# Kernel tuning notes

Measured on AMD Instinct MI355X. Metric: run time of the kernel, lower is better.

Reference implementation:

```python
import jax, jax.numpy as jnp
import numpy as np

CLAMP = 60.0
EPS = 1e-4

def _make_weights(N, alpha_logits, delta_logits, beta_logits):
    alpha = jax.nn.sigmoid(alpha_logits)   # [C,H]
    delta = jax.nn.sigmoid(delta_logits)
    beta = jax.nn.sigmoid(beta_logits)
    A = alpha * beta                        # [C,H]
    r = jnp.clip(1.0 - alpha * delta, EPS, 1.0 - EPS)
    t = jnp.arange(N, dtype=jnp.float32)[:, None, None]   # [N,1,1]
    logr = jnp.clip(jnp.log(r) * t, -CLAMP, CLAMP)        # [N,C,H]
    return A, jnp.exp(logr), jnp.exp(-logr)

def _ema_fwd(x, A, eta, r_pos, r_neg):
    # x: [B,N,C] -> y: [B,N,C]
    z = A * x[..., None] * r_neg            # [B,N,C,H]
    h = jnp.cumsum(z, axis=1) * r_pos       # [B,N,C,H]
    return jnp.sum(eta * h, axis=-1)        # [B,N,C]

def reference(x, alpha_logits, delta_logits, beta_logits, eta, proj_w, proj_b):
    B, N, C = x.shape
    A, r_pos, r_neg = _make_weights(N, alpha_logits, delta_logits, beta_logits)
    xf = x.astype(jnp.float32)
    y_fwd = _ema_fwd(xf, A, eta, r_pos, r_neg)
    y_bwd = _ema_fwd(xf[:, ::-1], A, eta, r_pos, r_neg)[:, ::-1]
    z = jnp.concatenate([y_fwd, y_bwd], axis=-1).astype(x.dtype)  # [B,N,2C]
    return z @ proj_w.T + proj_b            # [B,N,C]

def setup_inputs():
    key = jax.random.key(0)
    ks = jax.random.split(key, 7)
    B, N, C, H = 8, 4096, 512, 4
    return {
        "x": jax.random.normal(ks[0], (B, N, C), dtype=jnp.float32),
        "alpha_logits": jax.random.normal(ks[1], (C, H), dtype=jnp.float32),
        "delta_logits": jax.random.normal(ks[2], (C, H), dtype=jnp.float32),
        "beta_logits": jax.random.normal(ks[3], (C, H), dtype=jnp.float32),
        "eta": jax.random.normal(ks[4], (C, H), dtype=jnp.float32) * 0.02,
        "proj_w": jax.random.normal(ks[5], (C, 2 * C), dtype=jnp.float32) / np.sqrt(2.0 * C),
        "proj_b": jax.random.normal(ks[6], (C,), dtype=jnp.float32) * 0.01,
    }
```

## Files before the change

kernel.cpp:

```cpp
#include <hip/hip_runtime.h>
#include <hip/hip_bf16.h>

#define B_ 8
#define N_ 4096
#define C_ 512
#define H_ 4
#define EPS_ 1e-4f
#define E60P 1.14200739e26f
#define E60M 8.7565108e-27f

typedef __attribute__((ext_vector_type(8))) short short8;
typedef __attribute__((ext_vector_type(4))) float floatx4;
typedef __attribute__((ext_vector_type(2))) float floatx2;
typedef unsigned short ushort_t;

__device__ __forceinline__ float sigmoidf_(float v) {
    return 1.0f / (1.0f + expf(-v));
}

__device__ __forceinline__ int pk_off(int t, int w, int k0, int ks, int f,
                                      int lane8, int kb) {
    return ((((t * 2 + w) * 16 + k0) * 2 + ks) * 4 + f) * 512 + lane8 * 8 + kb;
}

__global__ __launch_bounds__(256) void k_partials3(
    const float* __restrict__ x, const float* __restrict__ al,
    const float* __restrict__ dl, const float* __restrict__ bl,
    float* __restrict__ P)
{
    int bid   = blockIdx.x;
    int chunk = bid & 15;
    int ct    = (bid >> 4) & 7;
    int b     = bid >> 7;
    int lane  = threadIdx.x & 63;
    int wave  = threadIdx.x >> 6;
    int c     = ct * 64 + lane;
    int sub   = chunk * 4 + wave;
    int t0f   = sub * 64;
    int t0b   = (63 - sub) * 64;

    float aa[4], dd[4], bb[4];
    { float4 v = ((const float4*)al)[c]; aa[0]=v.x; aa[1]=v.y; aa[2]=v.z; aa[3]=v.w; }
    { float4 v = ((const float4*)dl)[c]; dd[0]=v.x; dd[1]=v.y; dd[2]=v.z; dd[3]=v.w; }
    { float4 v = ((const float4*)bl)[c]; bb[0]=v.x; bb[1]=v.y; bb[2]=v.z; bb[3]=v.w; }

    float A[H_], ri[H_], Lh[H_];
    #pragma unroll
    for (int h = 0; h < H_; ++h) {
        float alpha = sigmoidf_(aa[h]);
        float delta = sigmoidf_(dd[h]);
        float beta  = sigmoidf_(bb[h]);
        A[h] = alpha * beta;
        float r = fminf(fmaxf(1.0f - alpha * delta, EPS_), 1.0f - EPS_);
        Lh[h] = logf(r);
        ri[h] = 1.0f / r;
    }
    const floatx2 E2P = {E60P, E60P};
    floatx2 A2[2]  = {{A[0],  A[1]},  {A[2],  A[3]}};
    floatx2 ri2[2] = {{ri[0], ri[1]}, {ri[2], ri[3]}};

    const float* xp = x + ((size_t)b * N_ + t0f) * C_ + c;

    floatx2 ep2[2], T2[2];
    #pragma unroll
    for (int p = 0; p < 2; ++p) {
        ep2[p] = (floatx2){expf(fminf(-Lh[2*p]   * (float)t0f, 60.0f)),
                           expf(fminf(-Lh[2*p+1] * (float)t0f, 60.0f))};
        T2[p]  = (floatx2){0.f, 0.f};
    }
    {
        float cur[8];
        #pragma unroll
        for (int j = 0; j < 8; ++j) cur[j] = xp[(size_t)j * C_];
        #pragma unroll 1
        for (int g = 0; g < 8; ++g) {
            float nxt[8];
            if (g < 7) {
                #pragma unroll
                for (int j = 0; j < 8; ++j)
                    nxt[j] = xp[(size_t)(g * 8 + 8 + j) * C_];
            }
            #pragma unroll
            for (int j = 0; j < 8; ++j) {
                floatx2 xv2 = {cur[j], cur[j]};
                #pragma unroll
                for (int p = 0; p < 2; ++p) {
                    T2[p] += (A2[p] * xv2) * ep2[p];
                    ep2[p] = __builtin_elementwise_min(ep2[p] * ri2[p], E2P);
                }
            }
            if (g < 7) {
                #pragma unroll
                for (int j = 0; j < 8; ++j) cur[j] = nxt[j];
            }
        }
        float* pp = P + ((size_t)b * 64 + sub) * (H_ * C_) + c;
        pp[0]      = T2[0].x;  pp[C_]     = T2[0].y;
        pp[2 * C_] = T2[1].x;  pp[3 * C_] = T2[1].y;
    }

    #pragma unroll
    for (int p = 0; p < 2; ++p) {
        ep2[p] = (floatx2){expf(fminf(-Lh[2*p]   * (float)t0b, 60.0f)),
                           expf(fminf(-Lh[2*p+1] * (float)t0b, 60.0f))};
        T2[p]  = (floatx2){0.f, 0.f};
    }
    {
        float cur[8];
        #pragma unroll
        for (int j = 0; j < 8; ++j) cur[j] = xp[(size_t)(63 - j) * C_];
        #pragma unroll 1
        for (int g = 0; g < 8; ++g) {
            float nxt[8];
            if (g < 7) {
                #pragma unroll
                for (int j = 0; j < 8; ++j)
                    nxt[j] = xp[(size_t)(63 - (g * 8 + 8 + j)) * C_];
            }
            #pragma unroll
            for (int j = 0; j < 8; ++j) {
                floatx2 xv2 = {cur[j], cur[j]};
                #pragma unroll
                for (int p = 0; p < 2; ++p) {
                    T2[p] += (A2[p] * xv2) * ep2[p];
                    ep2[p] = __builtin_elementwise_min(ep2[p] * ri2[p], E2P);
                }
            }
            if (g < 7) {
                #pragma unroll
                for (int j = 0; j < 8; ++j) cur[j] = nxt[j];
            }
        }
        float* pp = P + ((size_t)(8 + b) * 64 + (63 - sub)) * (H_ * C_) + c;
        pp[0]      = T2[0].x;  pp[C_]     = T2[0].y;
        pp[2 * C_] = T2[1].x;  pp[3 * C_] = T2[1].y;
    }
}

__global__ __launch_bounds__(256) void k_scan(float* __restrict__ P)
{
    int bid = blockIdx.x;
    int ct  = bid & 7;
    int b   = (bid >> 3) & 7;
    int dir = bid >> 6;
    int cl  = threadIdx.x & 63;
    int h   = threadIdx.x >> 6;
    int c   = ct * 64 + cl;

    float run = 0.0f;
    float* base = P + ((size_t)(dir * 8 + b) * 64) * (H_ * C_) + h * C_ + c;
    for (int s = 0; s < 64; ++s) {
        float v = base[s * (H_ * C_)];
        base[s * (H_ * C_)] = run;
        run += v;
    }
}

__global__ __launch_bounds__(256) void k_apply3(
    const float* __restrict__ x, const float* __restrict__ al,
    const float* __restrict__ dl, const float* __restrict__ bl,
    const float* __restrict__ eta, const float* __restrict__ P,
    ushort_t* __restrict__ Zp)
{
    int bid   = blockIdx.x;
    int chunk = bid & 15;
    int ct    = (bid >> 4) & 7;
    int b     = bid >> 7;
    int lane  = threadIdx.x & 63;
    int wave  = threadIdx.x >> 6;
    int c     = ct * 64 + lane;
    int sub   = chunk * 4 + wave;
    int t0f   = sub * 64;
    int t0b   = (63 - sub) * 64;

    int ksv = lane >> 5, qv = (lane >> 3) & 3, kbv = lane & 7;
    int mt  = b * 32 + (t0f >> 7);
    int wq  = (t0f >> 6) & 1;
    int offcF = pk_off(mt, wq, ct,     ksv, 0, qv * 16, kbv);
    int offcB = pk_off(mt, wq, 8 + ct, ksv, 0, qv * 16, kbv);

    float aa[4], dd[4], bb[4], ee[4];
    { float4 v = ((const float4*)al )[c]; aa[0]=v.x; aa[1]=v.y; aa[2]=v.z; aa[3]=v.w; }
    { float4 v = ((const float4*)dl )[c]; dd[0]=v.x; dd[1]=v.y; dd[2]=v.z; dd[3]=v.w; }
    { float4 v = ((const float4*)bl )[c]; bb[0]=v.x; bb[1]=v.y; bb[2]=v.z; bb[3]=v.w; }
    { float4 v = ((const float4*)eta)[c]; ee[0]=v.x; ee[1]=v.y; ee[2]=v.z; ee[3]=v.w; }

    float A[H_], rr[H_], ri[H_], Lh[H_];
    #pragma unroll
    for (int h = 0; h < H_; ++h) {
        float alpha = sigmoidf_(aa[h]);
        float delta = sigmoidf_(dd[h]);
        float beta  = sigmoidf_(bb[h]);
        A[h] = alpha * beta;
        float r = fminf(fmaxf(1.0f - alpha * delta, EPS_), 1.0f - EPS_);
        Lh[h] = logf(r);
        rr[h] = r;
        ri[h] = 1.0f / r;
    }
    const floatx2 E2P = {E60P, E60P};
    const floatx2 E2M = {E60M, E60M};
    floatx2 A2[2]  = {{A[0],  A[1]},  {A[2],  A[3]}};
    floatx2 ri2[2] = {{ri[0], ri[1]}, {ri[2], ri[3]}};
    floatx2 rr2[2] = {{rr[0], rr[1]}, {rr[2], rr[3]}};
    floatx2 ee2[2] = {{ee[0], ee[1]}, {ee[2], ee[3]}};

    const float* xp = x + ((size_t)b * N_ + t0f) * C_ + c;

    {
        const float* cp = P + ((size_t)b * 64 + sub) * (H_ * C_) + c;
        floatx2 ep2[2], em2[2], S2[2];
        #pragma unroll
        for (int p = 0; p < 2; ++p) {
            ep2[p] = (floatx2){expf(fminf(-Lh[2*p]   * (float)t0f, 60.0f)),
                               expf(fminf(-Lh[2*p+1] * (float)t0f, 60.0f))};
            em2[p] = (floatx2){expf(fmaxf( Lh[2*p]   * (float)t0f, -60.0f)),
                               expf(fmaxf( Lh[2*p+1] * (float)t0f, -60.0f))};
            S2[p]  = (floatx2){cp[(2*p) * C_], cp[(2*p+1) * C_]};
        }
        float cur[8];
        #pragma unroll
        for (int j = 0; j < 8; ++j) cur[j] = xp[(size_t)j * C_];
        #pragma unroll 1
        for (int g = 0; g < 8; ++g) {
            float nxt[8];
            if (g < 7) {
                #pragma unroll
                for (int j = 0; j < 8; ++j)
                    nxt[j] = xp[(size_t)(g * 8 + 8 + j) * C_];
            }
            #pragma unroll
            for (int j = 0; j < 8; ++j) {
                int i = g * 8 + j;
                floatx2 xv2 = {cur[j], cur[j]};
                floatx2 acc = {0.f, 0.f};
                #pragma unroll
                for (int p = 0; p < 2; ++p) {
                    S2[p] += (A2[p] * xv2) * ep2[p];
                    ep2[p] = __builtin_elementwise_min(ep2[p] * ri2[p], E2P);
                    acc   += ee2[p] * (em2[p] * S2[p]);
                    em2[p] = __builtin_elementwise_max(em2[p] * rr2[p], E2M);
                }
                float y = acc.x + acc.y;
                __hip_bfloat16 yb = __float2bfloat16(y);
                Zp[offcF + (i >> 4) * 512 + (i & 15) * 8] = *(ushort_t*)&yb;
            }
            if (g < 7) {
                #pragma unroll
                for (int j = 0; j < 8; ++j) cur[j] = nxt[j];
            }
        }
    }

    {
        const float* cp = P + ((size_t)(8 + b) * 64 + (63 - sub)) * (H_ * C_) + c;
        floatx2 ep2[2], em2[2], S2[2];
        #pragma unroll
        for (int p = 0; p < 2; ++p) {
            ep2[p] = (floatx2){expf(fminf(-Lh[2*p]   * (float)t0b, 60.0f)),
                               expf(fminf(-Lh[2*p+1] * (float)t0b, 60.0f))};
            em2[p] = (floatx2){expf(fmaxf( Lh[2*p]   * (float)t0b, -60.0f)),
                               expf(fmaxf( Lh[2*p+1] * (float)t0b, -60.0f))};
            S2[p]  = (floatx2){cp[(2*p) * C_], cp[(2*p+1) * C_]};
        }
        float cur[8];
        #pragma unroll
        for (int j = 0; j < 8; ++j) cur[j] = xp[(size_t)(63 - j) * C_];
        #pragma unroll 1
        for (int g = 0; g < 8; ++g) {
            float nxt[8];
            if (g < 7) {
                #pragma unroll
                for (int j = 0; j < 8; ++j)
                    nxt[j] = xp[(size_t)(63 - (g * 8 + 8 + j)) * C_];
            }
            #pragma unroll
            for (int j = 0; j < 8; ++j) {
                int i = 63 - (g * 8 + j);
                floatx2 xv2 = {cur[j], cur[j]};
                floatx2 acc = {0.f, 0.f};
                #pragma unroll
                for (int p = 0; p < 2; ++p) {
                    S2[p] += (A2[p] * xv2) * ep2[p];
                    ep2[p] = __builtin_elementwise_min(ep2[p] * ri2[p], E2P);
                    acc   += ee2[p] * (em2[p] * S2[p]);
                    em2[p] = __builtin_elementwise_max(em2[p] * rr2[p], E2M);
                }
                float y = acc.x + acc.y;
                __hip_bfloat16 yb = __float2bfloat16(y);
                Zp[offcB + (i >> 4) * 512 + (i & 15) * 8] = *(ushort_t*)&yb;
            }
            if (g < 7) {
                #pragma unroll
                for (int j = 0; j < 8; ++j) cur[j] = nxt[j];
            }
        }
    }
}

__global__ __launch_bounds__(256) void k_cvtw2(const float* __restrict__ w,
                                               ushort_t* __restrict__ Wp)
{
    int i = blockIdx.x * 256 + threadIdx.x;
    int n = i >> 10, k = i & 1023;
    int nt = n >> 7, rn = n & 127;
    int k0 = k >> 6, kk = k & 63;
    int off = pk_off(nt, rn >> 6, k0, kk >> 5, (rn >> 4) & 3,
                     ((kk >> 3) & 3) * 16 + (rn & 15), kk & 7);
    __hip_bfloat16 vb = __float2bfloat16(w[i]);
    Wp[off] = *(ushort_t*)&vb;
}

__global__ __launch_bounds__(256, 2) void k_gemm2(
    const ushort_t* __restrict__ Zp, const ushort_t* __restrict__ Wp,
    const float* __restrict__ bias, float* __restrict__ out)
{
    __shared__ __align__(16) float stg[32 * 132];

    int tid  = threadIdx.x;
    int lane = tid & 63, wave = tid >> 6;
    int wm   = wave & 1, wn = wave >> 1;
    int fr   = lane & 15, quad = lane >> 4;

    int bid = blockIdx.x;
    int mt  = ((bid >> 5) << 3) | (bid & 7);
    int nt  = (bid >> 3) & 3;
    int m0  = mt * 128, n0 = nt * 128;

    const ushort_t* Ab = Zp + ((size_t)(mt * 2 + wm) * 16) * 4096 + lane * 8;
    const ushort_t* Bb = Wp + ((size_t)(nt * 2 + wn) * 16) * 4096 + lane * 8;

    floatx4 acc[4][4];
    #pragma unroll
    for (int mf = 0; mf < 4; ++mf)
        #pragma unroll
        for (int nf = 0; nf < 4; ++nf)
            acc[mf][nf] = (floatx4){0.f, 0.f, 0.f, 0.f};

    #pragma unroll
    for (int k0 = 0; k0 < 16; ++k0) {
        short8 af[2][4], bf[2][4];
        #pragma unroll
        for (int ks = 0; ks < 2; ++ks)
            #pragma unroll
            for (int f = 0; f < 4; ++f) {
                af[ks][f] = *(const short8*)(Ab + k0 * 4096 + (ks * 4 + f) * 512);
                bf[ks][f] = *(const short8*)(Bb + k0 * 4096 + (ks * 4 + f) * 512);
            }
        #pragma unroll
        for (int ks = 0; ks < 2; ++ks)
            #pragma unroll
            for (int mf = 0; mf < 4; ++mf)
                #pragma unroll
                for (int nf = 0; nf < 4; ++nf)
                    acc[mf][nf] = __builtin_amdgcn_mfma_f32_16x16x32_bf16(
                        af[ks][mf], bf[ks][nf], acc[mf][nf], 0, 0, 0);
    }

    int rrow = tid >> 3;
    int seg  = tid & 7;
    int gcol = n0 + seg * 16;

    #pragma unroll
    for (int ch = 0; ch < 4; ++ch) {
        if ((wave & 1) == (ch >> 1)) {
            int ml = (ch & 1) * 2;
            #pragma unroll
            for (int mi = 0; mi < 2; ++mi) {
                #pragma unroll
                for (int nf = 0; nf < 4; ++nf) {
                    int col = wn * 64 + nf * 16 + fr;
                    #pragma unroll
                    for (int rg = 0; rg < 4; ++rg) {
                        int row = mi * 16 + quad * 4 + rg;
                        stg[row * 132 + col] = acc[ml + mi][nf][rg];
                    }
                }
            }
        }
        __syncthreads();
        {
            int gm = m0 + ch * 32 + rrow;
            const float* s = &stg[rrow * 132 + seg * 16];
            #pragma unroll
            for (int k = 0; k < 4; ++k) {
                float4 v  = *(const float4*)&s[k * 4];
                float4 bv = *(const float4*)&bias[gcol + k * 4];
                v.x += bv.x; v.y += bv.y; v.z += bv.z; v.w += bv.w;
                *(float4*)&out[(size_t)gm * 512 + gcol + k * 4] = v;
            }
        }
        __syncthreads();
    }
}

extern "C" void kernel_launch(void* const* d_in, const int* in_sizes, int n_in,
                              void* d_out, int out_size, void* d_ws, size_t ws_size,
                              hipStream_t stream)
{
    const float* x  = (const float*)d_in[0];
    const float* al = (const float*)d_in[1];
    const float* dl = (const float*)d_in[2];
    const float* bl = (const float*)d_in[3];
    const float* et = (const float*)d_in[4];
    const float* pw = (const float*)d_in[5];
    const float* pb = (const float*)d_in[6];
    float* out = (float*)d_out;

    ushort_t* Zp = (ushort_t*)d_ws;
    float*    P  = (float*)((char*)d_ws + 67108864);
    ushort_t* Wp = (ushort_t*)((char*)d_ws + 75497472);

    hipLaunchKernelGGL(k_cvtw2,     dim3(2048), dim3(256), 0, stream, pw, Wp);
    hipLaunchKernelGGL(k_partials3, dim3(1024), dim3(256), 0, stream, x, al, dl, bl, P);
    hipLaunchKernelGGL(k_scan,      dim3(128),  dim3(256), 0, stream, P);
    hipLaunchKernelGGL(k_apply3,    dim3(1024), dim3(256), 0, stream, x, al, dl, bl, et, P, Zp);
    hipLaunchKernelGGL(k_gemm2,     dim3(1024), dim3(256), 0, stream, Zp, Wp, pb, out);
}
```

Baseline: 225.1 us.

## Stage GEMM operands via global_load_lds, vectorize weight convert, batch scan loads

The GEMM now copies each K-slab of A and B into shared memory with direct global-to-LDS loads, so each tile is fetched once per block rather than once per wave. It synchronizes twice per K-step and raises the occupancy hint to 4 blocks per CU. The weight conversion kernel now handles four elements per thread with float4 loads and 64-bit stores. The scan kernel loads all 64 partials into registers before running the prefix sum, which removes the serialized load-store dependency. Single-buffered LDS staging with a full vmcnt wait can expose memory latency, since no copy overlaps the MFMA work.

```diff
diff --git a/kernel.cpp b/kernel.cpp
--- a/kernel.cpp
+++ b/kernel.cpp
@@ -12,6 +12,7 @@
 typedef __attribute__((ext_vector_type(8))) short short8;
 typedef __attribute__((ext_vector_type(4))) float floatx4;
 typedef __attribute__((ext_vector_type(2))) float floatx2;
+typedef __attribute__((ext_vector_type(4))) unsigned short ushort4_t;
 typedef unsigned short ushort_t;
 
 __device__ __forceinline__ float sigmoidf_(float v) {
@@ -21,6 +22,12 @@
 __device__ __forceinline__ int pk_off(int t, int w, int k0, int ks, int f,
                                       int lane8, int kb) {
     return ((((t * 2 + w) * 16 + k0) * 2 + ks) * 4 + f) * 512 + lane8 * 8 + kb;
+}
+
+__device__ __forceinline__ void gload16(const void* g, void* l) {
+    __builtin_amdgcn_global_load_lds(
+        (const __attribute__((address_space(1))) void*)g,
+        (__attribute__((address_space(3))) void*)l, 16, 0, 0);
 }
 
 __global__ __launch_bounds__(256) void k_partials3(
@@ -147,13 +154,18 @@
     int h   = threadIdx.x >> 6;
     int c   = ct * 64 + cl;
 
+    float* base = P + ((size_t)(dir * 8 + b) * 64) * (H_ * C_) + h * C_ + c;
+
+    float v[64];
+    #pragma unroll
+    for (int s = 0; s < 64; ++s) v[s] = base[s * (H_ * C_)];
+
     float run = 0.0f;
-    float* base = P + ((size_t)(dir * 8 + b) * 64) * (H_ * C_) + h * C_ + c;
-    for (int s = 0; s < 64; ++s) {
-        float v = base[s * (H_ * C_)];
-        base[s * (H_ * C_)] = run;
-        run += v;
-    }
+    #pragma unroll
+    for (int s = 0; s < 64; ++s) { float t = v[s]; v[s] = run; run += t; }
+
+    #pragma unroll
+    for (int s = 0; s < 64; ++s) base[s * (H_ * C_)] = v[s];
 }
 
 __global__ __launch_bounds__(256) void k_apply3(
@@ -300,21 +312,30 @@
 __global__ __launch_bounds__(256) void k_cvtw2(const float* __restrict__ w,
                                                ushort_t* __restrict__ Wp)
 {
-    int i = blockIdx.x * 256 + threadIdx.x;
+    int i4 = blockIdx.x * 256 + threadIdx.x;
+    int i  = i4 << 2;
     int n = i >> 10, k = i & 1023;
     int nt = n >> 7, rn = n & 127;
     int k0 = k >> 6, kk = k & 63;
     int off = pk_off(nt, rn >> 6, k0, kk >> 5, (rn >> 4) & 3,
                      ((kk >> 3) & 3) * 16 + (rn & 15), kk & 7);
-    __hip_bfloat16 vb = __float2bfloat16(w[i]);
-    Wp[off] = *(ushort_t*)&vb;
-}
-
-__global__ __launch_bounds__(256, 2) void k_gemm2(
+    float4 v = ((const float4*)w)[i4];
+    ushort4_t r;
+    { __hip_bfloat16 t = __float2bfloat16(v.x); r.x = *(ushort_t*)&t; }
+    { __hip_bfloat16 t = __float2bfloat16(v.y); r.y = *(ushort_t*)&t; }
+    { __hip_bfloat16 t = __float2bfloat16(v.z); r.z = *(ushort_t*)&t; }
+    { __hip_bfloat16 t = __float2bfloat16(v.w); r.w = *(ushort_t*)&t; }
+    *(ushort4_t*)&Wp[off] = r;
+}
+
+__global__ __launch_bounds__(256, 4) void k_gemm3(
     const ushort_t* __restrict__ Zp, const ushort_t* __restrict__ Wp,
     const float* __restrict__ bias, float* __restrict__ out)
 {
-    __shared__ __align__(16) float stg[32 * 132];
+    __shared__ __align__(16) char lds[32768];
+    char*  ldsA = lds;
+    char*  ldsB = lds + 16384;
+    float* stg  = (float*)lds;
 
     int tid  = threadIdx.x;
     int lane = tid & 63, wave = tid >> 6;
@@ -326,8 +347,8 @@
     int nt  = (bid >> 3) & 3;
     int m0  = mt * 128, n0 = nt * 128;
 
-    const ushort_t* Ab = Zp + ((size_t)(mt * 2 + wm) * 16) * 4096 + lane * 8;
-    const ushort_t* Bb = Wp + ((size_t)(nt * 2 + wn) * 16) * 4096 + lane * 8;
+    const ushort_t* Az = Zp + ((size_t)(mt * 2) * 16) * 4096;
+    const ushort_t* Bz = Wp + ((size_t)(nt * 2) * 16) * 4096;
 
     floatx4 acc[4][4];
     #pragma unroll
@@ -336,24 +357,37 @@
         for (int nf = 0; nf < 4; ++nf)
             acc[mf][nf] = (floatx4){0.f, 0.f, 0.f, 0.f};
 
-    #pragma unroll
     for (int k0 = 0; k0 < 16; ++k0) {
-        short8 af[2][4], bf[2][4];
-        #pragma unroll
-        for (int ks = 0; ks < 2; ++ks)
+        const ushort_t* As = Az + (size_t)k0 * 4096;
+        const ushort_t* Bs = Bz + (size_t)k0 * 4096;
+        #pragma unroll
+        for (int w = 0; w < 2; ++w)
+            #pragma unroll
+            for (int inst = 0; inst < 2; ++inst) {
+                gload16(As + w * 65536 + inst * 2048 + tid * 8,
+                        ldsA + w * 8192 + inst * 4096 + tid * 16);
+                gload16(Bs + w * 65536 + inst * 2048 + tid * 8,
+                        ldsB + w * 8192 + inst * 4096 + tid * 16);
+            }
+        asm volatile("s_waitcnt vmcnt(0)" ::: "memory");
+        __syncthreads();
+
+        #pragma unroll
+        for (int ks = 0; ks < 2; ++ks) {
+            short8 af[4], bf[4];
             #pragma unroll
             for (int f = 0; f < 4; ++f) {
-                af[ks][f] = *(const short8*)(Ab + k0 * 4096 + (ks * 4 + f) * 512);
-                bf[ks][f] = *(const short8*)(Bb + k0 * 4096 + (ks * 4 + f) * 512);
-            }
-        #pragma unroll
-        for (int ks = 0; ks < 2; ++ks)
+                af[f] = *(const short8*)(ldsA + wm * 8192 + (ks * 4 + f) * 1024 + lane * 16);
+                bf[f] = *(const short8*)(ldsB + wn * 8192 + (ks * 4 + f) * 1024 + lane * 16);
+            }
             #pragma unroll
             for (int mf = 0; mf < 4; ++mf)
                 #pragma unroll
                 for (int nf = 0; nf < 4; ++nf)
                     acc[mf][nf] = __builtin_amdgcn_mfma_f32_16x16x32_bf16(
-                        af[ks][mf], bf[ks][nf], acc[mf][nf], 0, 0, 0);
+                        af[mf], bf[nf], acc[mf][nf], 0, 0, 0);
+        }
+        __syncthreads();
     }
 
     int rrow = tid >> 3;
@@ -410,9 +444,9 @@
     float*    P  = (float*)((char*)d_ws + 67108864);
     ushort_t* Wp = (ushort_t*)((char*)d_ws + 75497472);
 
-    hipLaunchKernelGGL(k_cvtw2,     dim3(2048), dim3(256), 0, stream, pw, Wp);
+    hipLaunchKernelGGL(k_cvtw2,     dim3(512),  dim3(256), 0, stream, pw, Wp);
     hipLaunchKernelGGL(k_partials3, dim3(1024), dim3(256), 0, stream, x, al, dl, bl, P);
     hipLaunchKernelGGL(k_scan,      dim3(128),  dim3(256), 0, stream, P);
     hipLaunchKernelGGL(k_apply3,    dim3(1024), dim3(256), 0, stream, x, al, dl, bl, et, P, Zp);
-    hipLaunchKernelGGL(k_gemm2,     dim3(1024), dim3(256), 0, stream, Zp, Wp, pb, out);
-}
+    hipLaunchKernelGGL(k_gemm3,     dim3(1024), dim3(256), 0, stream, Zp, Wp, pb, out);
+}
```

Result: no change. 224.8 us (-0.1%).
